# Kernel tuning notes

Hardware: AMD Instinct MI355X
Metric: run time of the kernel (lower is better)

The kernel has to match this reference:

```python
import jax, jax.numpy as jnp
import numpy as np

IMG = 224
BLK = 8
POOL = 7


def dct_matrix(n=BLK):
    # Orthonormal DCT-II matrix: dct(v, norm='ortho') == D @ v
    k = jnp.arange(n, dtype=jnp.float32)[:, None]
    m = jnp.arange(n, dtype=jnp.float32)[None, :]
    D = jnp.cos(jnp.pi * (2.0 * m + 1.0) * k / (2.0 * n)) * jnp.sqrt(2.0 / n)
    return D.at[0].mul(1.0 / jnp.sqrt(2.0))


def conv3x3(x, w, b):
    # NCHW, OIHW, stride 1, SAME padding
    y = jax.lax.conv_general_dilated(x, w, (1, 1), 'SAME',
                                     dimension_numbers=('NCHW', 'OIHW', 'NCHW'))
    return y + b[None, :, None, None]


def adaptive_pool7(x):
    # [B,C,224,224] -> [B,C,7,7] via mean over 32x32 windows
    B, C, H, W = x.shape
    return x.reshape(B, C, POOL, H // POOL, POOL, W // POOL).mean(axis=(3, 5))


def setup_inputs() -> dict:
    key = jax.random.key(0)
    ks = jax.random.split(key, 7)
    B = 32
    x = jax.random.uniform(ks[0], (B, 3, IMG, IMG), dtype=jnp.float32)
    s = 0.02
    return {
        'x': x,
        'dct_w': jax.random.normal(ks[1], (64, 3, 3, 3), jnp.float32) * s,
        'dct_b': jnp.zeros((64,), jnp.float32),
        'fft_w': jax.random.normal(ks[2], (64, 6, 3, 3), jnp.float32) * s,
        'fft_b': jnp.zeros((64,), jnp.float32),
        'fc_w': jax.random.normal(ks[3], (512, 2 * 64 * POOL * POOL), jnp.float32) * s,
        'fc_b': jnp.zeros((512,), jnp.float32),
    }


def reference(x, dct_w, dct_b, fft_w, fft_b, fc_w, fc_b):
    B = x.shape[0]
    # ---- DCT branch ----
    # grayscale (RGB2GRAY) scaled to 0..255 (uint8 cast omitted for differentiability)
    gray = (0.299 * x[:, 0] + 0.587 * x[:, 1] + 0.114 * x[:, 2]) * 255.0  # [B,H,W]
    nb = (IMG - BLK) // BLK  # 27: loop range(0, H-8, 8) skips the last block row/col
    g = gray[:, :nb * BLK, :nb * BLK].reshape(B, nb, BLK, nb, BLK)
    blocks = g.transpose(0, 1, 3, 2, 4).reshape(B, nb * nb, BLK, BLK)
    D = dct_matrix()
    dct_blocks = jnp.einsum('ij,bnjk,lk->bnil', D, blocks, D)  # 2D ortho DCT per block
    dct_img = dct_blocks.mean(axis=1)  # [B,8,8]
    dct_resized = jax.image.resize(dct_img, (B, IMG, IMG), method='linear')
    dct_in = jnp.broadcast_to(dct_resized[:, None], (B, 3, IMG, IMG))
    dct_pooled = adaptive_pool7(conv3x3(dct_in, dct_w, dct_b)).reshape(B, -1)

    # ---- FFT branch ----
    f = jnp.fft.fft2(x)  # [B,3,H,W] complex
    # channel order: real0, imag0, real1, imag1, real2, imag2
    fft_in = jnp.stack([f.real.astype(jnp.float32), f.imag.astype(jnp.float32)],
                       axis=2).reshape(B, 6, IMG, IMG)
    fft_pooled = adaptive_pool7(conv3x3(fft_in, fft_w, fft_b)).reshape(B, -1)

    combined = jnp.concatenate([dct_pooled, fft_pooled], axis=1)  # [B,6272]
    return jax.nn.relu(combined @ fc_w.T + fc_b)
```

## Files before the change

### kernel.cpp

```cpp
#include <hip/hip_runtime.h>
#include <math.h>

#define IMG 224
#define NR  21

__device__ __forceinline__ void range_lohi(int r, int& lo, int& hi) {
    int py = r / 3, s = (r % 3) - 1;
    lo = 32 * py + s; hi = lo + 32;
    if (lo < 0) lo = 0;
    if (hi > IMG) hi = IMG;
}

__device__ __forceinline__ float2 geom_range(int lo, int len, int y,
                                             const float* c0, const float* s0) {
    if (y == 0) return make_float2((float)len, 0.f);
    int i0 = (lo * y) % IMG;
    int iL = (len * y) % IMG;
    float w0x = c0[i0], w0y = s0[i0];
    float wLx = c0[iL], wLy = s0[iL];
    float w1x = c0[y],  w1y = s0[y];
    float nx = w0x * (1.f - wLx) + w0y * wLy;
    float ny = w0y * (1.f - wLx) - w0x * wLy;
    float dx = 1.f - w1x, dy = -w1y;
    float inv = 1.f / (dx * dx + dy * dy);
    return make_float2((nx * dx + ny * dy) * inv, (ny * dx - nx * dy) * inv);
}

__device__ __forceinline__ void build_cis(float* c0, float* s0, int t) {
    if (t < IMG) {
        double ang = 2.0 * M_PI * (double)t / (double)IMG;
        c0[t] = (float)cos(ang);
        s0[t] = (float)(-sin(ang));
    }
}

__global__ __launch_bounds__(256) void k0_tab(float* __restrict__ are,
                                              float* __restrict__ aim)
{
    __shared__ float c0[IMG], s0[IMG];
    int t = threadIdx.x;
    build_cis(c0, s0, t);
    __syncthreads();
    int r = blockIdx.x;
    int lo, hi; range_lohi(r, lo, hi);
    if (t < 116) {
        float2 a = (t < 113) ? geom_range(lo, hi - lo, t, c0, s0)
                             : make_float2(0.f, 0.f);
        are[r * 116 + t] = a.x;
        aim[r * 116 + t] = a.y;
    }
}

__global__ __launch_bounds__(256) void ka_rowdft_gray(const float* __restrict__ x,
        const float* __restrict__ dct_w,
        const float* __restrict__ are, const float* __restrict__ aim,
        float2* __restrict__ T, float* __restrict__ meansum,
        float* __restrict__ afold_g, float* __restrict__ Dm_g,
        float* __restrict__ wsum3_g)
{
    __shared__ __align__(16) char smem[32256];
    int t = threadIdx.x;
    int blk = blockIdx.x;

    if (blk < 336) {
        int part = __builtin_amdgcn_readfirstlane((t >> 6) & 3);
        int lane = t & 63;
        int row = blk * 64 + lane;
        const float* src = x + (size_t)row * IMG;
        int base0 = part * 28;

        float sv[28], dv[28];
        #pragma unroll
        for (int ci = 0; ci < 7; ++ci) {
            int base = base0 + 4 * ci;
            float4 f = *(const float4*)(src + base);
            float fj[4] = { f.x, f.y, f.z, f.w };
            #pragma unroll
            for (int j = 0; j < 4; ++j) {
                int n = base + j;
                float xm = (n == 0) ? 0.f : src[IMG - n];
                sv[4 * ci + j] = fj[j] + xm;
                dv[4 * ci + j] = fj[j] - xm;
            }
        }
        float x112 = src[112];

        float2 acc[NR];
        for (int c = 0; c < NR; ++c) {
            const float* arp = are + c * 116 + base0;
            const float* aip = aim + c * 116 + base0;
            float re = 0.f, im = 0.f;
            #pragma unroll
            for (int ci = 0; ci < 7; ++ci) {
                float4 a4 = *(const float4*)(arp + 4 * ci);
                float4 b4 = *(const float4*)(aip + 4 * ci);
                re += sv[4*ci+0]*a4.x + sv[4*ci+1]*a4.y + sv[4*ci+2]*a4.z + sv[4*ci+3]*a4.w;
                im += dv[4*ci+0]*b4.x + dv[4*ci+1]*b4.y + dv[4*ci+2]*b4.z + dv[4*ci+3]*b4.w;
            }
            if (part == 0) {
                re += x112 * arp[112];
                im += x112 * aip[112];
            }
            acc[c] = make_float2(re, im);
        }

        float2* red = (float2*)smem;
        if (part > 0) {
            float2* dst = red + ((size_t)(part - 1) * 64 + lane) * NR;
            #pragma unroll
            for (int c = 0; c < NR; ++c) dst[c] = acc[c];
        }
        __syncthreads();
        if (part == 0) {
            #pragma unroll
            for (int c = 0; c < NR; ++c) {
                float2 s = acc[c];
                float2 p1 = red[((size_t)0 * 64 + lane) * NR + c];
                float2 p2 = red[((size_t)1 * 64 + lane) * NR + c];
                float2 p3 = red[((size_t)2 * 64 + lane) * NR + c];
                s.x += p1.x + p2.x + p3.x;
                s.y += p1.y + p2.y + p3.y;
                T[(size_t)row * NR + c] = s;
            }
        }
    } else if (blk < 592) {
        int bb = blk - 336;
        int b = bb >> 3, j = bb & 7;
        float* sm = (float*)smem;
        if (t < 216) {
            const float* pr = x + (size_t)(b * 3 + 0) * IMG * IMG;
            const float* pg = x + (size_t)(b * 3 + 1) * IMG * IMG;
            const float* pb = x + (size_t)(b * 3 + 2) * IMG * IMG;
            float acc = 0.f;
            for (int by = 0; by < 27; ++by) {
                int o = (8 * by + j) * IMG + t;
                acc += 76.245f * pr[o] + 149.685f * pg[o] + 29.07f * pb[o];
            }
            sm[t] = acc;
        }
        __syncthreads();
        if (t < 8) {
            float s = 0.f;
            for (int q = t; q < 216; q += 8) s += sm[q];
            meansum[(b * 8 + j) * 8 + t] = s;
        }
    } else {
        if (t < NR * 8) {
            int r = t / 8, j = t % 8;
            int lo, hi; range_lohi(r, lo, hi);
            double s = 0.0;
            for (int y = lo; y < hi; ++y) {
                double sf = (y + 0.5) / 28.0 - 0.5;
                double w = 1.0 - fabs(sf - (double)j);
                if (w < 0.0) w = 0.0;
                double tot = 0.0;
                for (int jj = 0; jj < 8; ++jj) {
                    double wj = 1.0 - fabs(sf - (double)jj);
                    if (wj > 0.0) tot += wj;
                }
                s += w / tot;
            }
            afold_g[t] = (float)s;
        }
        if (t >= 192 && t < 256) {
            int i = t - 192, k = i / 8, m = i % 8;
            double v = cos(M_PI * (2.0 * m + 1.0) * k / 16.0) * 0.5;
            if (k == 0) v *= 0.70710678118654752440;
            Dm_g[i] = (float)v;
        }
        for (int i = t; i < 64 * 9; i += 256) {
            int cout = i / 9, q = i % 9;
            float s = 0.f;
            for (int cin = 0; cin < 3; ++cin) s += dct_w[(cout * 3 + cin) * 9 + q];
            wsum3_g[i] = s;
        }
    }
}

__global__ __launch_bounds__(256) void kb_fold(const float2* __restrict__ T,
        float2* __restrict__ rs2)
{
    __shared__ __align__(16) char smem[39424];
    float*  c0  = (float*)smem;
    float*  s0  = c0 + IMG;
    float2* sAh = (float2*)(smem + 1792);
    float2* sT  = (float2*)(smem + 20608);

    int blk = blockIdx.x, t = threadIdx.x;
    int b = blk / 6, rem = blk % 6;
    int cin = rem >> 1, half = rem & 1;

    build_cis(c0, s0, t);
    __syncthreads();
    for (int i = t; i < NR * 112; i += 256) {
        int rr = i / 112, y = half * 112 + (i % 112);
        int lo, hi; range_lohi(rr, lo, hi);
        sAh[i] = geom_range(lo, hi - lo, y, c0, s0);
    }
    const float2* Tbase = T + ((size_t)(b * 3 + cin) * IMG + half * 112) * NR;
    for (int i = t; i < 112 * NR; i += 256) sT[i] = Tbase[i];
    __syncthreads();

    float2* dst = rs2 + (size_t)((b * 3 + cin) * 2 + half) * NR * NR;
    for (int p = t; p < NR * NR; p += 256) {
        int rr = p / NR, cc = p % NR;
        float re = 0.f, im = 0.f;
        const float2* arow = &sAh[rr * 112];
        for (int y = 0; y < 112; ++y) {
            float2 a  = arow[y];
            float2 tv = sT[y * NR + cc];
            re += a.x * tv.x - a.y * tv.y;
            im += a.x * tv.y + a.y * tv.x;
        }
        dst[p] = make_float2(re, im);
    }
}

__global__ __launch_bounds__(256) void kb_asm(const float2* __restrict__ rs2,
        const float* __restrict__ meansum, const float* __restrict__ afold_g,
        const float* __restrict__ Dm_g, const float* __restrict__ wsum3_g,
        const float* __restrict__ dct_b, const float* __restrict__ fft_w,
        const float* __restrict__ fft_b, float* __restrict__ PT)
{
    __shared__ __align__(16) char smem[24576];
    int blk = blockIdx.x, t = threadIdx.x;
    int b = blk >> 1, which = blk & 1;
    const float inv = 1.0f / 1024.0f;

    if (which == 0) {
        float* WSd  = (float*)smem;
        float* Msc  = WSd + 441;
        float* dimg = Msc + 64;
        float* Ds   = dimg + 64;
        float* af   = Ds + 64;
        float* sws  = af + 168;
        if (t < 64) { Ds[t] = Dm_g[t]; Msc[t] = meansum[b * 64 + t] * (1.0f / 729.0f); }
        if (t < NR * 8) af[t] = afold_g[t];
        for (int i = t; i < 64 * 9; i += 256) sws[i] = wsum3_g[i];
        __syncthreads();
        if (t < 64) {
            int i = t / 8, l = t % 8;
            float s = 0.f;
            for (int j = 0; j < 8; ++j) {
                float rj = 0.f;
                for (int k = 0; k < 8; ++k) rj += Msc[j * 8 + k] * Ds[l * 8 + k];
                s += Ds[i * 8 + j] * rj;
            }
            dimg[t] = s;
        }
        __syncthreads();
        for (int p = t; p < NR * NR; p += 256) {
            int rr = p / NR, cc = p % NR;
            float s = 0.f;
            for (int j = 0; j < 8; ++j) {
                float rj = 0.f;
                for (int k = 0; k < 8; ++k) rj += dimg[j * 8 + k] * af[cc * 8 + k];
                s += af[rr * 8 + j] * rj;
            }
            WSd[p] = s;
        }
        __syncthreads();
        for (int i = t; i < 3136; i += 256) {
            int cout = i / 49, q = i % 49, py = q / 7, px = q % 7;
            float s = 0.f;
            #pragma unroll
            for (int ky = 0; ky < 3; ++ky)
                #pragma unroll
                for (int kx = 0; kx < 3; ++kx)
                    s += sws[cout * 9 + ky * 3 + kx] * WSd[(py * 3 + ky) * NR + (px * 3 + kx)];
            PT[(size_t)i * 32 + b] = dct_b[cout] + s * inv;
        }
    } else {
        float2* RSs = (float2*)smem;
        float*  sfw = (float*)(smem + 10584);
        for (int i = t; i < 3 * NR * NR; i += 256) {
            int cin = i / (NR * NR), p = i % (NR * NR);
            float2 v0 = rs2[(size_t)((b * 3 + cin) * 2 + 0) * NR * NR + p];
            float2 v1 = rs2[(size_t)((b * 3 + cin) * 2 + 1) * NR * NR + p];
            RSs[i] = make_float2(v0.x + v1.x, v0.y + v1.y);
        }
        for (int i = t; i < 64 * 6 * 9; i += 256) sfw[i] = fft_w[i];
        __syncthreads();
        for (int i = t; i < 3136; i += 256) {
            int cout = i / 49, q = i % 49, py = q / 7, px = q % 7;
            float s = 0.f;
            for (int cin = 0; cin < 3; ++cin) {
                #pragma unroll
                for (int ky = 0; ky < 3; ++ky)
                    #pragma unroll
                    for (int kx = 0; kx < 3; ++kx) {
                        float2 v = RSs[cin * NR * NR + (py * 3 + ky) * NR + (px * 3 + kx)];
                        const float* wp = &sfw[(cout * 6 + 2 * cin) * 9 + ky * 3 + kx];
                        s += wp[0] * v.x + wp[9] * v.y;
                    }
            }
            PT[(size_t)(3136 + i) * 32 + b] = fft_b[cout] + s * inv;
        }
    }
}

__global__ __launch_bounds__(256) void kc_fc(const float* __restrict__ PT,
        const float* __restrict__ fc_w, float* __restrict__ part)
{
    int oc = blockIdx.x / 14;
    int kc = blockIdx.x % 14;
    int t = threadIdx.x;
    int b = t & 31, sub = t >> 5;
    int o0 = oc * 4;
    int k0 = kc * 448 + sub * 56;

    const float* w0 = fc_w + (size_t)(o0 + 0) * 6272 + k0;
    const float* w1 = fc_w + (size_t)(o0 + 1) * 6272 + k0;
    const float* w2 = fc_w + (size_t)(o0 + 2) * 6272 + k0;
    const float* w3 = fc_w + (size_t)(o0 + 3) * 6272 + k0;
    const float* p  = PT + (size_t)k0 * 32 + b;

    float a0 = 0.f, a1 = 0.f, a2 = 0.f, a3 = 0.f;
    #pragma unroll 2
    for (int k = 0; k < 56; k += 4) {
        float4 v0 = *(const float4*)(w0 + k);
        float4 v1 = *(const float4*)(w1 + k);
        float4 v2 = *(const float4*)(w2 + k);
        float4 v3 = *(const float4*)(w3 + k);
        float p0 = p[(k + 0) * 32];
        float p1 = p[(k + 1) * 32];
        float p2 = p[(k + 2) * 32];
        float p3 = p[(k + 3) * 32];
        a0 += p0 * v0.x + p1 * v0.y + p2 * v0.z + p3 * v0.w;
        a1 += p0 * v1.x + p1 * v1.y + p2 * v1.z + p3 * v1.w;
        a2 += p0 * v2.x + p1 * v2.y + p2 * v2.z + p3 * v2.w;
        a3 += p0 * v3.x + p1 * v3.y + p2 * v3.z + p3 * v3.w;
    }

    __shared__ float sm[8 * 128];
    sm[sub * 128 +  0 + b] = a0;
    sm[sub * 128 + 32 + b] = a1;
    sm[sub * 128 + 64 + b] = a2;
    sm[sub * 128 + 96 + b] = a3;
    __syncthreads();
    if (t < 128) {
        int oi = t >> 5, b2 = t & 31;
        float s = 0.f;
        #pragma unroll
        for (int c = 0; c < 8; ++c) s += sm[c * 128 + oi * 32 + b2];
        part[(size_t)kc * 16384 + (size_t)(o0 + oi) * 32 + b2] = s;
    }
}

__global__ __launch_bounds__(256) void kc_out(const float* __restrict__ part,
        const float* __restrict__ fc_b, float* __restrict__ out)
{
    int idx = blockIdx.x * 256 + threadIdx.x;
    int o = idx >> 5, b = idx & 31;
    float s = fc_b[o];
    #pragma unroll
    for (int c = 0; c < 14; ++c) s += part[(size_t)c * 16384 + idx];
    out[(size_t)b * 512 + o] = fmaxf(s, 0.f);
}

extern "C" void kernel_launch(void* const* d_in, const int* in_sizes, int n_in,
                              void* d_out, int out_size, void* d_ws, size_t ws_size,
                              hipStream_t stream)
{
    const float* x     = (const float*)d_in[0];
    const float* dct_w = (const float*)d_in[1];
    const float* dct_b = (const float*)d_in[2];
    const float* fft_w = (const float*)d_in[3];
    const float* fft_b = (const float*)d_in[4];
    const float* fc_w  = (const float*)d_in[5];
    const float* fc_b  = (const float*)d_in[6];
    float* out = (float*)d_out;

    char* ws = (char*)d_ws;
    size_t off = 0;
    auto alloc = [&](size_t bytes) {
        char* p = ws + off;
        off = (off + bytes + 255) & ~(size_t)255;
        return p;
    };
    float2* T       = (float2*)alloc((size_t)21504 * NR * 8);
    float*  are     = (float*) alloc((size_t)NR * 116 * 4);
    float*  aim     = (float*) alloc((size_t)NR * 116 * 4);
    float*  meansum = (float*) alloc(32 * 64 * 4);
    float*  afold_g = (float*) alloc(NR * 8 * 4);
    float*  Dm_g    = (float*) alloc(64 * 4);
    float*  wsum3_g = (float*) alloc(64 * 9 * 4);
    float2* rs2     = (float2*)alloc((size_t)192 * NR * NR * 8);
    float*  PT      = (float*) alloc((size_t)6272 * 32 * 4);
    float*  part    = (float*) alloc((size_t)14 * 512 * 32 * 4);
    (void)ws_size; (void)in_sizes; (void)n_in; (void)out_size;

    hipLaunchKernelGGL(k0_tab,         dim3(21),   dim3(256), 0, stream, are, aim);
    hipLaunchKernelGGL(ka_rowdft_gray, dim3(593),  dim3(256), 0, stream,
                       x, dct_w, are, aim, T, meansum, afold_g, Dm_g, wsum3_g);
    hipLaunchKernelGGL(kb_fold,        dim3(192),  dim3(256), 0, stream, T, rs2);
    hipLaunchKernelGGL(kb_asm,         dim3(64),   dim3(256), 0, stream,
                       rs2, meansum, afold_g, Dm_g, wsum3_g, dct_b, fft_w, fft_b, PT);
    hipLaunchKernelGGL(kc_fc,          dim3(1792), dim3(256), 0, stream, PT, fc_w, part);
    hipLaunchKernelGGL(kc_out,         dim3(64),   dim3(256), 0, stream, part, fc_b, out);
}
```

Measured before the change: 143.5 us.

## Fuse fold+assemble and fc+output kernels using last-block atomic counters

Merges kb_fold with kb_asm, and kc_fc with kc_out. In each merged kernel the last block to arrive, found through an atomic counter with threadfences, does the follow-on work, which removes two kernel launches. The constant-table setup moves from ka into k0_tab, which also zeroes the counters. The cost is that the DCT and FFT assembly now run serially in one block per batch instead of two parallel blocks, and the fused kernels carry atomic and fence overhead.

```diff
diff --git a/kernel.cpp b/kernel.cpp
--- a/kernel.cpp
+++ b/kernel.cpp
@@ -34,117 +34,25 @@
     }
 }
 
-__global__ __launch_bounds__(256) void k0_tab(float* __restrict__ are,
-                                              float* __restrict__ aim)
+__global__ __launch_bounds__(256) void k0_tab(const float* __restrict__ dct_w,
+        float* __restrict__ are, float* __restrict__ aim,
+        float* __restrict__ afold_g, float* __restrict__ Dm_g,
+        float* __restrict__ wsum3_g, int* __restrict__ cnt)
 {
-    __shared__ float c0[IMG], s0[IMG];
-    int t = threadIdx.x;
-    build_cis(c0, s0, t);
-    __syncthreads();
-    int r = blockIdx.x;
-    int lo, hi; range_lohi(r, lo, hi);
-    if (t < 116) {
-        float2 a = (t < 113) ? geom_range(lo, hi - lo, t, c0, s0)
-                             : make_float2(0.f, 0.f);
-        are[r * 116 + t] = a.x;
-        aim[r * 116 + t] = a.y;
-    }
-}
-
-__global__ __launch_bounds__(256) void ka_rowdft_gray(const float* __restrict__ x,
-        const float* __restrict__ dct_w,
-        const float* __restrict__ are, const float* __restrict__ aim,
-        float2* __restrict__ T, float* __restrict__ meansum,
-        float* __restrict__ afold_g, float* __restrict__ Dm_g,
-        float* __restrict__ wsum3_g)
-{
-    __shared__ __align__(16) char smem[32256];
-    int t = threadIdx.x;
-    int blk = blockIdx.x;
-
-    if (blk < 336) {
-        int part = __builtin_amdgcn_readfirstlane((t >> 6) & 3);
-        int lane = t & 63;
-        int row = blk * 64 + lane;
-        const float* src = x + (size_t)row * IMG;
-        int base0 = part * 28;
-
-        float sv[28], dv[28];
-        #pragma unroll
-        for (int ci = 0; ci < 7; ++ci) {
-            int base = base0 + 4 * ci;
-            float4 f = *(const float4*)(src + base);
-            float fj[4] = { f.x, f.y, f.z, f.w };
-            #pragma unroll
-            for (int j = 0; j < 4; ++j) {
-                int n = base + j;
-                float xm = (n == 0) ? 0.f : src[IMG - n];
-                sv[4 * ci + j] = fj[j] + xm;
-                dv[4 * ci + j] = fj[j] - xm;
-            }
-        }
-        float x112 = src[112];
-
-        float2 acc[NR];
-        for (int c = 0; c < NR; ++c) {
-            const float* arp = are + c * 116 + base0;
-            const float* aip = aim + c * 116 + base0;
-            float re = 0.f, im = 0.f;
-            #pragma unroll
-            for (int ci = 0; ci < 7; ++ci) {
-                float4 a4 = *(const float4*)(arp + 4 * ci);
-                float4 b4 = *(const float4*)(aip + 4 * ci);
-                re += sv[4*ci+0]*a4.x + sv[4*ci+1]*a4.y + sv[4*ci+2]*a4.z + sv[4*ci+3]*a4.w;
-                im += dv[4*ci+0]*b4.x + dv[4*ci+1]*b4.y + dv[4*ci+2]*b4.z + dv[4*ci+3]*b4.w;
-            }
-            if (part == 0) {
-                re += x112 * arp[112];
-                im += x112 * aip[112];
-            }
-            acc[c] = make_float2(re, im);
-        }
-
-        float2* red = (float2*)smem;
-        if (part > 0) {
-            float2* dst = red + ((size_t)(part - 1) * 64 + lane) * NR;
-            #pragma unroll
-            for (int c = 0; c < NR; ++c) dst[c] = acc[c];
-        }
+    int t = threadIdx.x, blk = blockIdx.x;
+    if (blk < NR) {
+        __shared__ float c0[IMG], s0[IMG];
+        build_cis(c0, s0, t);
         __syncthreads();
-        if (part == 0) {
-            #pragma unroll
-            for (int c = 0; c < NR; ++c) {
-                float2 s = acc[c];
-                float2 p1 = red[((size_t)0 * 64 + lane) * NR + c];
-                float2 p2 = red[((size_t)1 * 64 + lane) * NR + c];
-                float2 p3 = red[((size_t)2 * 64 + lane) * NR + c];
-                s.x += p1.x + p2.x + p3.x;
-                s.y += p1.y + p2.y + p3.y;
-                T[(size_t)row * NR + c] = s;
-            }
-        }
-    } else if (blk < 592) {
-        int bb = blk - 336;
-        int b = bb >> 3, j = bb & 7;
-        float* sm = (float*)smem;
-        if (t < 216) {
-            const float* pr = x + (size_t)(b * 3 + 0) * IMG * IMG;
-            const float* pg = x + (size_t)(b * 3 + 1) * IMG * IMG;
-            const float* pb = x + (size_t)(b * 3 + 2) * IMG * IMG;
-            float acc = 0.f;
-            for (int by = 0; by < 27; ++by) {
-                int o = (8 * by + j) * IMG + t;
-                acc += 76.245f * pr[o] + 149.685f * pg[o] + 29.07f * pb[o];
-            }
-            sm[t] = acc;
-        }
-        __syncthreads();
-        if (t < 8) {
-            float s = 0.f;
-            for (int q = t; q < 216; q += 8) s += sm[q];
-            meansum[(b * 8 + j) * 8 + t] = s;
-        }
-    } else {
+        int r = blk;
+        int lo, hi; range_lohi(r, lo, hi);
+        if (t < 116) {
+            float2 a = (t < 113) ? geom_range(lo, hi - lo, t, c0, s0)
+                                 : make_float2(0.f, 0.f);
+            are[r * 116 + t] = a.x;
+            aim[r * 116 + t] = a.y;
+        }
+    } else if (blk == NR) {
         if (t < NR * 8) {
             int r = t / 8, j = t % 8;
             int lo, hi; range_lohi(r, lo, hi);
@@ -174,13 +82,113 @@
             for (int cin = 0; cin < 3; ++cin) s += dct_w[(cout * 3 + cin) * 9 + q];
             wsum3_g[i] = s;
         }
-    }
-}
-
-__global__ __launch_bounds__(256) void kb_fold(const float2* __restrict__ T,
-        float2* __restrict__ rs2)
+    } else {
+        if (t < 160) cnt[t] = 0;
+    }
+}
+
+__global__ __launch_bounds__(256) void ka_rowdft_gray(const float* __restrict__ x,
+        const float* __restrict__ are, const float* __restrict__ aim,
+        float2* __restrict__ T, float* __restrict__ meansum)
+{
+    __shared__ __align__(16) char smem[32256];
+    int t = threadIdx.x;
+    int blk = blockIdx.x;
+
+    if (blk < 336) {
+        int part = __builtin_amdgcn_readfirstlane((t >> 6) & 3);
+        int lane = t & 63;
+        int row = blk * 64 + lane;
+        const float* src = x + (size_t)row * IMG;
+        int base0 = part * 28;
+
+        float sv[28], dv[28];
+        #pragma unroll
+        for (int ci = 0; ci < 7; ++ci) {
+            int base = base0 + 4 * ci;
+            float4 f = *(const float4*)(src + base);
+            float fj[4] = { f.x, f.y, f.z, f.w };
+            #pragma unroll
+            for (int j = 0; j < 4; ++j) {
+                int n = base + j;
+                float xm = (n == 0) ? 0.f : src[IMG - n];
+                sv[4 * ci + j] = fj[j] + xm;
+                dv[4 * ci + j] = fj[j] - xm;
+            }
+        }
+        float x112 = src[112];
+
+        float2 acc[NR];
+        for (int c = 0; c < NR; ++c) {
+            const float* arp = are + c * 116 + base0;
+            const float* aip = aim + c * 116 + base0;
+            float re = 0.f, im = 0.f;
+            #pragma unroll
+            for (int ci = 0; ci < 7; ++ci) {
+                float4 a4 = *(const float4*)(arp + 4 * ci);
+                float4 b4 = *(const float4*)(aip + 4 * ci);
+                re += sv[4*ci+0]*a4.x + sv[4*ci+1]*a4.y + sv[4*ci+2]*a4.z + sv[4*ci+3]*a4.w;
+                im += dv[4*ci+0]*b4.x + dv[4*ci+1]*b4.y + dv[4*ci+2]*b4.z + dv[4*ci+3]*b4.w;
+            }
+            if (part == 0) {
+                re += x112 * arp[112];
+                im += x112 * aip[112];
+            }
+            acc[c] = make_float2(re, im);
+        }
+
+        float2* red = (float2*)smem;
+        if (part > 0) {
+            float2* dst = red + ((size_t)(part - 1) * 64 + lane) * NR;
+            #pragma unroll
+            for (int c = 0; c < NR; ++c) dst[c] = acc[c];
+        }
+        __syncthreads();
+        if (part == 0) {
+            #pragma unroll
+            for (int c = 0; c < NR; ++c) {
+                float2 s = acc[c];
+                float2 p1 = red[((size_t)0 * 64 + lane) * NR + c];
+                float2 p2 = red[((size_t)1 * 64 + lane) * NR + c];
+                float2 p3 = red[((size_t)2 * 64 + lane) * NR + c];
+                s.x += p1.x + p2.x + p3.x;
+                s.y += p1.y + p2.y + p3.y;
+                T[(size_t)row * NR + c] = s;
+            }
+        }
+    } else {
+        int bb = blk - 336;
+        int b = bb >> 3, j = bb & 7;
+        float* sm = (float*)smem;
+        if (t < 216) {
+            const float* pr = x + (size_t)(b * 3 + 0) * IMG * IMG;
+            const float* pg = x + (size_t)(b * 3 + 1) * IMG * IMG;
+            const float* pb = x + (size_t)(b * 3 + 2) * IMG * IMG;
+            float acc = 0.f;
+            for (int by = 0; by < 27; ++by) {
+                int o = (8 * by + j) * IMG + t;
+                acc += 76.245f * pr[o] + 149.685f * pg[o] + 29.07f * pb[o];
+            }
+            sm[t] = acc;
+        }
+        __syncthreads();
+        if (t < 8) {
+            float s = 0.f;
+            for (int q = t; q < 216; q += 8) s += sm[q];
+            meansum[(b * 8 + j) * 8 + t] = s;
+        }
+    }
+}
+
+__global__ __launch_bounds__(256) void kb_fused(const float2* __restrict__ T,
+        float2* __restrict__ rs2, const float* __restrict__ meansum,
+        const float* __restrict__ afold_g, const float* __restrict__ Dm_g,
+        const float* __restrict__ wsum3_g, const float* __restrict__ dct_b,
+        const float* __restrict__ fft_w, const float* __restrict__ fft_b,
+        float* __restrict__ PT, int* __restrict__ cnt)
 {
     __shared__ __align__(16) char smem[39424];
+    __shared__ int isLast;
     float*  c0  = (float*)smem;
     float*  s0  = c0 + IMG;
     float2* sAh = (float2*)(smem + 1792);
@@ -214,93 +222,89 @@
         }
         dst[p] = make_float2(re, im);
     }
-}
-
-__global__ __launch_bounds__(256) void kb_asm(const float2* __restrict__ rs2,
-        const float* __restrict__ meansum, const float* __restrict__ afold_g,
-        const float* __restrict__ Dm_g, const float* __restrict__ wsum3_g,
-        const float* __restrict__ dct_b, const float* __restrict__ fft_w,
-        const float* __restrict__ fft_b, float* __restrict__ PT)
-{
-    __shared__ __align__(16) char smem[24576];
-    int blk = blockIdx.x, t = threadIdx.x;
-    int b = blk >> 1, which = blk & 1;
+
+    __threadfence();
+    __syncthreads();
+    if (t == 0) isLast = (atomicAdd(&cnt[b], 1) == 5);
+    __syncthreads();
+    if (!isLast) return;
+    __threadfence();
+
+    float2* RSs = (float2*)smem;
+    float*  WSd = (float*)(smem + 10584);
+    float*  sfw = (float*)(smem + 10584 + 1764);
+    float*  Msc = (float*)(smem + 10584 + 1764 + 13824);
+    float*  dimg = Msc + 64;
+    float*  Ds   = dimg + 64;
+    float*  af   = Ds + 64;
+    float*  sws  = af + 168;
+
+    for (int i = t; i < 3 * NR * NR; i += 256) {
+        int ci2 = i / (NR * NR), p = i % (NR * NR);
+        float2 v0 = rs2[(size_t)((b * 3 + ci2) * 2 + 0) * NR * NR + p];
+        float2 v1 = rs2[(size_t)((b * 3 + ci2) * 2 + 1) * NR * NR + p];
+        RSs[i] = make_float2(v0.x + v1.x, v0.y + v1.y);
+    }
+    if (t < 64) { Ds[t] = Dm_g[t]; Msc[t] = meansum[b * 64 + t] * (1.0f / 729.0f); }
+    if (t >= 64 && t < 64 + NR * 8) af[t - 64] = afold_g[t - 64];
+    for (int i = t; i < 64 * 6 * 9; i += 256) sfw[i] = fft_w[i];
+    for (int i = t; i < 64 * 9; i += 256) sws[i] = wsum3_g[i];
+    __syncthreads();
+    if (t < 64) {
+        int i = t / 8, l = t % 8;
+        float s = 0.f;
+        for (int j = 0; j < 8; ++j) {
+            float rj = 0.f;
+            for (int k = 0; k < 8; ++k) rj += Msc[j * 8 + k] * Ds[l * 8 + k];
+            s += Ds[i * 8 + j] * rj;
+        }
+        dimg[t] = s;
+    }
+    __syncthreads();
+    for (int p = t; p < NR * NR; p += 256) {
+        int rr = p / NR, cc = p % NR;
+        float s = 0.f;
+        for (int j = 0; j < 8; ++j) {
+            float rj = 0.f;
+            for (int k = 0; k < 8; ++k) rj += dimg[j * 8 + k] * af[cc * 8 + k];
+            s += af[rr * 8 + j] * rj;
+        }
+        WSd[p] = s;
+    }
+    __syncthreads();
+
     const float inv = 1.0f / 1024.0f;
-
-    if (which == 0) {
-        float* WSd  = (float*)smem;
-        float* Msc  = WSd + 441;
-        float* dimg = Msc + 64;
-        float* Ds   = dimg + 64;
-        float* af   = Ds + 64;
-        float* sws  = af + 168;
-        if (t < 64) { Ds[t] = Dm_g[t]; Msc[t] = meansum[b * 64 + t] * (1.0f / 729.0f); }
-        if (t < NR * 8) af[t] = afold_g[t];
-        for (int i = t; i < 64 * 9; i += 256) sws[i] = wsum3_g[i];
-        __syncthreads();
-        if (t < 64) {
-            int i = t / 8, l = t % 8;
-            float s = 0.f;
-            for (int j = 0; j < 8; ++j) {
-                float rj = 0.f;
-                for (int k = 0; k < 8; ++k) rj += Msc[j * 8 + k] * Ds[l * 8 + k];
-                s += Ds[i * 8 + j] * rj;
-            }
-            dimg[t] = s;
-        }
-        __syncthreads();
-        for (int p = t; p < NR * NR; p += 256) {
-            int rr = p / NR, cc = p % NR;
-            float s = 0.f;
-            for (int j = 0; j < 8; ++j) {
-                float rj = 0.f;
-                for (int k = 0; k < 8; ++k) rj += dimg[j * 8 + k] * af[cc * 8 + k];
-                s += af[rr * 8 + j] * rj;
-            }
-            WSd[p] = s;
-        }
-        __syncthreads();
-        for (int i = t; i < 3136; i += 256) {
-            int cout = i / 49, q = i % 49, py = q / 7, px = q % 7;
-            float s = 0.f;
+    for (int i = t; i < 3136; i += 256) {
+        int cout = i / 49, q = i % 49, py = q / 7, px = q % 7;
+        float s = 0.f;
+        #pragma unroll
+        for (int ky = 0; ky < 3; ++ky)
+            #pragma unroll
+            for (int kx = 0; kx < 3; ++kx)
+                s += sws[cout * 9 + ky * 3 + kx] * WSd[(py * 3 + ky) * NR + (px * 3 + kx)];
+        PT[(size_t)i * 32 + b] = dct_b[cout] + s * inv;
+    }
+    for (int i = t; i < 3136; i += 256) {
+        int cout = i / 49, q = i % 49, py = q / 7, px = q % 7;
+        float s = 0.f;
+        for (int ci2 = 0; ci2 < 3; ++ci2) {
             #pragma unroll
             for (int ky = 0; ky < 3; ++ky)
                 #pragma unroll
-                for (int kx = 0; kx < 3; ++kx)
-                    s += sws[cout * 9 + ky * 3 + kx] * WSd[(py * 3 + ky) * NR + (px * 3 + kx)];
-            PT[(size_t)i * 32 + b] = dct_b[cout] + s * inv;
-        }
-    } else {
-        float2* RSs = (float2*)smem;
-        float*  sfw = (float*)(smem + 10584);
-        for (int i = t; i < 3 * NR * NR; i += 256) {
-            int cin = i / (NR * NR), p = i % (NR * NR);
-            float2 v0 = rs2[(size_t)((b * 3 + cin) * 2 + 0) * NR * NR + p];
-            float2 v1 = rs2[(size_t)((b * 3 + cin) * 2 + 1) * NR * NR + p];
-            RSs[i] = make_float2(v0.x + v1.x, v0.y + v1.y);
-        }
-        for (int i = t; i < 64 * 6 * 9; i += 256) sfw[i] = fft_w[i];
-        __syncthreads();
-        for (int i = t; i < 3136; i += 256) {
-            int cout = i / 49, q = i % 49, py = q / 7, px = q % 7;
-            float s = 0.f;
-            for (int cin = 0; cin < 3; ++cin) {
-                #pragma unroll
-                for (int ky = 0; ky < 3; ++ky)
-                    #pragma unroll
-                    for (int kx = 0; kx < 3; ++kx) {
-                        float2 v = RSs[cin * NR * NR + (py * 3 + ky) * NR + (px * 3 + kx)];
-                        const float* wp = &sfw[(cout * 6 + 2 * cin) * 9 + ky * 3 + kx];
-                        s += wp[0] * v.x + wp[9] * v.y;
-                    }
-            }
-            PT[(size_t)(3136 + i) * 32 + b] = fft_b[cout] + s * inv;
-        }
-    }
-}
-
-__global__ __launch_bounds__(256) void kc_fc(const float* __restrict__ PT,
-        const float* __restrict__ fc_w, float* __restrict__ part)
+                for (int kx = 0; kx < 3; ++kx) {
+                    float2 v = RSs[ci2 * NR * NR + (py * 3 + ky) * NR + (px * 3 + kx)];
+                    const float* wp = &sfw[(cout * 6 + 2 * ci2) * 9 + ky * 3 + kx];
+                    s += wp[0] * v.x + wp[9] * v.y;
+                }
+        }
+        PT[(size_t)(3136 + i) * 32 + b] = fft_b[cout] + s * inv;
+    }
+}
+
+__global__ __launch_bounds__(256) void kc_fused(const float* __restrict__ PT,
+        const float* __restrict__ fc_w, const float* __restrict__ fc_b,
+        float* __restrict__ part, int* __restrict__ cnt,
+        float* __restrict__ out)
 {
     int oc = blockIdx.x / 14;
     int kc = blockIdx.x % 14;
@@ -333,6 +337,7 @@
     }
 
     __shared__ float sm[8 * 128];
+    __shared__ int isLast;
     sm[sub * 128 +  0 + b] = a0;
     sm[sub * 128 + 32 + b] = a1;
     sm[sub * 128 + 64 + b] = a2;
@@ -345,17 +350,20 @@
         for (int c = 0; c < 8; ++c) s += sm[c * 128 + oi * 32 + b2];
         part[(size_t)kc * 16384 + (size_t)(o0 + oi) * 32 + b2] = s;
     }
-}
-
-__global__ __launch_bounds__(256) void kc_out(const float* __restrict__ part,
-        const float* __restrict__ fc_b, float* __restrict__ out)
-{
-    int idx = blockIdx.x * 256 + threadIdx.x;
-    int o = idx >> 5, b = idx & 31;
-    float s = fc_b[o];
-    #pragma unroll
-    for (int c = 0; c < 14; ++c) s += part[(size_t)c * 16384 + idx];
-    out[(size_t)b * 512 + o] = fmaxf(s, 0.f);
+    __threadfence();
+    __syncthreads();
+    if (t == 0) isLast = (atomicAdd(&cnt[oc], 1) == 13);
+    __syncthreads();
+    if (!isLast) return;
+    __threadfence();
+    if (t < 128) {
+        int oi = t >> 5, b2 = t & 31;
+        float s = fc_b[o0 + oi];
+        #pragma unroll
+        for (int c = 0; c < 14; ++c)
+            s += part[(size_t)c * 16384 + (size_t)(o0 + oi) * 32 + b2];
+        out[(size_t)b2 * 512 + o0 + oi] = fmaxf(s, 0.f);
+    }
 }
 
 extern "C" void kernel_launch(void* const* d_in, const int* in_sizes, int n_in,
@@ -388,14 +396,16 @@
     float2* rs2     = (float2*)alloc((size_t)192 * NR * NR * 8);
     float*  PT      = (float*) alloc((size_t)6272 * 32 * 4);
     float*  part    = (float*) alloc((size_t)14 * 512 * 32 * 4);
+    int*    cnt     = (int*)   alloc(160 * 4);
     (void)ws_size; (void)in_sizes; (void)n_in; (void)out_size;
 
-    hipLaunchKernelGGL(k0_tab,         dim3(21),   dim3(256), 0, stream, are, aim);
-    hipLaunchKernelGGL(ka_rowdft_gray, dim3(593),  dim3(256), 0, stream,
-                       x, dct_w, are, aim, T, meansum, afold_g, Dm_g, wsum3_g);
-    hipLaunchKernelGGL(kb_fold,        dim3(192),  dim3(256), 0, stream, T, rs2);
-    hipLaunchKernelGGL(kb_asm,         dim3(64),   dim3(256), 0, stream,
-                       rs2, meansum, afold_g, Dm_g, wsum3_g, dct_b, fft_w, fft_b, PT);
-    hipLaunchKernelGGL(kc_fc,          dim3(1792), dim3(256), 0, stream, PT, fc_w, part);
-    hipLaunchKernelGGL(kc_out,         dim3(64),   dim3(256), 0, stream, part, fc_b, out);
-}
+    hipLaunchKernelGGL(k0_tab,         dim3(23),   dim3(256), 0, stream,
+                       dct_w, are, aim, afold_g, Dm_g, wsum3_g, cnt);
+    hipLaunchKernelGGL(ka_rowdft_gray, dim3(592),  dim3(256), 0, stream,
+                       x, are, aim, T, meansum);
+    hipLaunchKernelGGL(kb_fused,       dim3(192),  dim3(256), 0, stream,
+                       T, rs2, meansum, afold_g, Dm_g, wsum3_g, dct_b, fft_w, fft_b,
+                       PT, cnt);
+    hipLaunchKernelGGL(kc_fused,       dim3(1792), dim3(256), 0, stream,
+                       PT, fc_w, fc_b, part, cnt + 32, out);
+}
```

After: 351.3 us. 2.45x slower.
